# Performance work log

Measured on AMD Instinct MI355X. Metric: run time of the kernel, lower is better.

The kernel has to match this reference:

```python
import jax, jax.numpy as jnp
import numpy as np

EMBED_DIM = 1024
NUM_HEADS = 16
HEAD_DIM = EMBED_DIM // NUM_HEADS
BSZ = 8
SEQ = 1024


def setup_inputs() -> dict:
    key = jax.random.key(0)
    ks = jax.random.split(key, 8)
    s = 1.0 / np.sqrt(EMBED_DIM)
    return {
        "query": jax.random.normal(ks[0], (BSZ, SEQ, EMBED_DIM), jnp.float32),
        "key": jax.random.normal(ks[1], (BSZ, SEQ, EMBED_DIM), jnp.float32),
        "value": jax.random.normal(ks[2], (BSZ, SEQ, EMBED_DIM), jnp.float32),
        "Wq": jax.random.normal(ks[3], (EMBED_DIM, EMBED_DIM), jnp.float32) * s,
        "bq": jnp.zeros((EMBED_DIM,), jnp.float32),
        "Wk": jax.random.normal(ks[4], (EMBED_DIM, EMBED_DIM), jnp.float32) * s,
        "bk": jnp.zeros((EMBED_DIM,), jnp.float32),
        "Wv": jax.random.normal(ks[5], (EMBED_DIM, EMBED_DIM), jnp.float32) * s,
        "bv": jnp.zeros((EMBED_DIM,), jnp.float32),
        "Wo": jax.random.normal(ks[6], (EMBED_DIM, EMBED_DIM), jnp.float32) * s,
        "bo": jnp.zeros((EMBED_DIM,), jnp.float32),
    }


def reference(query, key, value, Wq, bq, Wk, bk, Wv, bv, Wo, bo):
    # B=0 path of hfta MultiheadAttention, dropout=0 (eval), no masks.
    bsz, tgt_len, embed_dim = query.shape
    src_len = key.shape[1]
    scaling = HEAD_DIM ** -0.5

    # torch Linear: y = x @ W.T + b
    q = (jnp.einsum('bte,fe->btf', query, Wq) + bq) * scaling
    k = jnp.einsum('bse,fe->bsf', key, Wk) + bk
    v = jnp.einsum('bse,fe->bsf', value, Wv) + bv

    # split heads: [b, h, t, d]
    q = q.reshape(bsz, tgt_len, NUM_HEADS, HEAD_DIM).transpose(0, 2, 1, 3)
    k = k.reshape(bsz, src_len, NUM_HEADS, HEAD_DIM).transpose(0, 2, 1, 3)
    v = v.reshape(bsz, src_len, NUM_HEADS, HEAD_DIM).transpose(0, 2, 1, 3)

    scores = jnp.einsum('bhtd,bhsd->bhts', q, k)          # [b,h,t,s]
    attn = jax.nn.softmax(scores, axis=-1)
    o = jnp.einsum('bhts,bhsd->bhtd', attn, v)            # [b,h,t,d]
    o = o.transpose(0, 2, 1, 3).reshape(bsz, tgt_len, embed_dim)
    o = jnp.einsum('bte,fe->btf', o, Wo) + bo
    return o
```

## Files before the change

kernel.cpp:

```cpp
#include <hip/hip_runtime.h>
#include <hip/hip_bf16.h>

#define BSZ   8
#define SEQ   1024
#define EMB   1024
#define NH    16
#define HD    64
#define MROWS (BSZ*SEQ)
#define LOG2E 1.44269504088896f

typedef short  short8  __attribute__((ext_vector_type(8)));
typedef short  short4v __attribute__((ext_vector_type(4)));
typedef float  floatx4 __attribute__((ext_vector_type(4)));
typedef unsigned int uint2v __attribute__((ext_vector_type(2)));
typedef unsigned int uint4v __attribute__((ext_vector_type(4)));

__device__ __forceinline__ unsigned short f2bf(float f) {
  union { float f; unsigned u; } v; v.f = f;
  unsigned r = v.u + 0x7FFFu + ((v.u >> 16) & 1u);
  return (unsigned short)(r >> 16);
}
__device__ __forceinline__ unsigned pk2bf(float a, float b) {
  __hip_bfloat162 t = __float22bfloat162_rn(make_float2(a, b));
  union { __hip_bfloat162 h; unsigned u; } c; c.h = t; return c.u;
}

__device__ __forceinline__ void g2lds16(const unsigned short* g, unsigned short* l) {
  __builtin_amdgcn_global_load_lds(
      (const __attribute__((address_space(1))) unsigned int*)g,
      (__attribute__((address_space(3))) unsigned int*)l, 16, 0, 0);
}

__global__ __launch_bounds__(256) void convert_w4(
    const float* __restrict__ w0, const float* __restrict__ w1,
    const float* __restrict__ w2, const float* __restrict__ w3,
    unsigned short* __restrict__ out, float qs)
{
  const int z = blockIdx.y;
  const float* w = (z == 0) ? w0 : (z == 1) ? w1 : (z == 2) ? w2 : w3;
  const float s = (z == 0) ? qs : 1.0f;
  int i = blockIdx.x * 256 + threadIdx.x;
  float4 f = ((const float4*)w)[i];
  short4v p;
  p.x = (short)f2bf(f.x * s); p.y = (short)f2bf(f.y * s);
  p.z = (short)f2bf(f.z * s); p.w = (short)f2bf(f.w * s);
  ((short4v*)(out + (size_t)z * EMB * EMB))[i] = p;
}

template<int QKV>
__global__ __launch_bounds__(256, 2) void gemm_k(
    const float* __restrict__ A0, const float* __restrict__ A1,
    const float* __restrict__ A2,
    const unsigned short* __restrict__ Abf,
    const unsigned short* __restrict__ Wbase,
    const float* __restrict__ b0, const float* __restrict__ b1,
    const float* __restrict__ b2, float qs,
    unsigned short* __restrict__ obf, float* __restrict__ of32)
{
  __shared__ __align__(16) unsigned short As[2][128 * 64];
  __shared__ __align__(16) unsigned short Ws[2][128 * 64];
  const int tid  = threadIdx.x;
  const int lane = tid & 63, wid = tid >> 6;
  const int z    = QKV ? blockIdx.z : 0;
  const int n0   = blockIdx.x * 128;
  const int m0   = blockIdx.y * 128;
  const int wm = (wid & 1) * 64, wn = (wid >> 1) * 64;
  const int quad = lane >> 4, ln = lane & 15, e3 = ln & 7;
  const int lrow = lane >> 3;
  const int lcol8 = ((lane & 7) ^ lrow) * 8;

  const unsigned short* W = Wbase + (size_t)z * EMB * EMB;
  const float* Af = QKV ? ((z == 0) ? A0 : (z == 1) ? A1 : A2) : (const float*)0;
  const int ar = tid >> 1;
  const int ac = (tid & 1) * 32;

  floatx4 acc[4][4] = {};
  float4 ax[8];

  if (QKV) {
    const float* src = Af + (size_t)(m0 + ar) * EMB + ac;
#pragma unroll
    for (int i = 0; i < 8; i++) ax[i] = *(const float4*)(src + i * 4);
  }
#pragma unroll
  for (int c = 0; c < 4; c++) {
    int r = wid * 32 + c * 8;
    g2lds16(W + (size_t)(n0 + r + lrow) * EMB + lcol8, &Ws[0][r * 64]);
    if (!QKV) g2lds16(Abf + (size_t)(m0 + r + lrow) * EMB + lcol8, &As[0][r * 64]);
  }
  if (QKV) {
#pragma unroll
    for (int i = 0; i < 4; i++) {
      uint4v u;
      u.x = pk2bf(ax[2*i].x, ax[2*i].y);     u.y = pk2bf(ax[2*i].z, ax[2*i].w);
      u.z = pk2bf(ax[2*i+1].x, ax[2*i+1].y); u.w = pk2bf(ax[2*i+1].z, ax[2*i+1].w);
      int ch = (4 * (tid & 1) + i) ^ (ar & 7);
      *(uint4v*)&As[0][ar * 64 + ch * 8] = u;
    }
  }

  const int NK = EMB / 64;
  for (int it = 0; it < NK; ++it) {
    __syncthreads();
    const int cb = it & 1, nb = (it + 1) & 1;
    if (it < NK - 1) {
      const int k1 = (it + 1) * 64;
      if (QKV) {
        const float* src = Af + (size_t)(m0 + ar) * EMB + k1 + ac;
#pragma unroll
        for (int i = 0; i < 8; i++) ax[i] = *(const float4*)(src + i * 4);
      }
#pragma unroll
      for (int c = 0; c < 4; c++) {
        int r = wid * 32 + c * 8;
        g2lds16(W + (size_t)(n0 + r + lrow) * EMB + k1 + lcol8, &Ws[nb][r * 64]);
        if (!QKV) g2lds16(Abf + (size_t)(m0 + r + lrow) * EMB + k1 + lcol8, &As[nb][r * 64]);
      }
    }
#pragma unroll
    for (int ks = 0; ks < 2; ks++) {
      short8 af[4], wf[4];
#pragma unroll
      for (int t = 0; t < 4; t++) {
        int pc = ((4 * ks + quad) ^ e3) * 8;
        af[t] = *(const short8*)&As[cb][(wm + t * 16 + ln) * 64 + pc];
        wf[t] = *(const short8*)&Ws[cb][(wn + t * 16 + ln) * 64 + pc];
      }
#pragma unroll
      for (int mi = 0; mi < 4; mi++)
#pragma unroll
        for (int ni = 0; ni < 4; ni++)
          acc[mi][ni] = __builtin_amdgcn_mfma_f32_16x16x32_bf16(
              af[mi], wf[ni], acc[mi][ni], 0, 0, 0);
    }
    if (QKV && it < NK - 1) {
#pragma unroll
      for (int i = 0; i < 4; i++) {
        uint4v u;
        u.x = pk2bf(ax[2*i].x, ax[2*i].y);     u.y = pk2bf(ax[2*i].z, ax[2*i].w);
        u.z = pk2bf(ax[2*i+1].x, ax[2*i+1].y); u.w = pk2bf(ax[2*i+1].z, ax[2*i+1].w);
        int ch = (4 * (tid & 1) + i) ^ (ar & 7);
        *(uint4v*)&As[nb][ar * 64 + ch * 8] = u;
      }
    }
  }

  const float* bias = QKV ? ((z == 0) ? b0 : (z == 1) ? b1 : b2) : b0;
  const float bsc = (QKV && z == 0) ? qs : 1.0f;
  unsigned short* outz = obf + (size_t)z * MROWS * EMB;

#pragma unroll
  for (int mi = 0; mi < 4; mi++) {
#pragma unroll
    for (int ni = 0; ni < 4; ni++) {
      int gn = n0 + wn + ni * 16 + ln;
      float bv = bsc * bias[gn];
      int gmb = m0 + wm + mi * 16 + quad * 4;
      if (!QKV) {
#pragma unroll
        for (int r = 0; r < 4; r++)
          of32[(size_t)(gmb + r) * EMB + gn] = acc[mi][ni][r] + bv;
      } else if (z < 2) {
        int h = gn >> 6, d = gn & 63;
#pragma unroll
        for (int r = 0; r < 4; r++) {
          int gm = gmb + r;
          int b = gm >> 10, s = gm & 1023;
          outz[((size_t)(b * NH + h) * SEQ + s) * HD + d] = f2bf(acc[mi][ni][r] + bv);
        }
      } else {
        int h = gn >> 6, d = gn & 63;
        int b = gmb >> 10, s = gmb & 1023;
        short4v pkt;
        pkt.x = (short)f2bf(acc[mi][ni][0] + bv);
        pkt.y = (short)f2bf(acc[mi][ni][1] + bv);
        pkt.z = (short)f2bf(acc[mi][ni][2] + bv);
        pkt.w = (short)f2bf(acc[mi][ni][3] + bv);
        *(short4v*)&outz[((size_t)(b * NH + h) * HD + d) * SEQ + s] = pkt;
      }
    }
  }
}

__global__ __launch_bounds__(256, 2) void attn_k(
    const unsigned short* __restrict__ q,
    const unsigned short* __restrict__ k,
    const unsigned short* __restrict__ vt,
    unsigned short* __restrict__ o)
{
  __shared__ __align__(16) unsigned short Ks[2][64 * 64];
  __shared__ __align__(16) unsigned short Vs[2][64 * 64];
  __shared__ __align__(16) unsigned short Pb[4][16][72];
  const int tid  = threadIdx.x;
  const int lane = tid & 63, wv = tid >> 6;
  const int quad = lane >> 4, ln = lane & 15, e3 = ln & 7;
  const int bh = blockIdx.x >> 2;
  const int tb = (blockIdx.x & 3) * 256;
  const int b = bh >> 4, h = bh & 15;
  const int lrow = lane >> 3;
  const int lcol8 = ((lane & 7) ^ lrow) * 8;

  const unsigned short* qh = q  + (size_t)bh * SEQ * HD;
  const unsigned short* kh = k  + (size_t)bh * SEQ * HD;
  const unsigned short* vh = vt + (size_t)bh * HD * SEQ;

  short8 qf[4][2];
#pragma unroll
  for (int tt = 0; tt < 4; tt++)
#pragma unroll
    for (int kc = 0; kc < 2; kc++)
      qf[tt][kc] = *(const short8*)(qh +
          (size_t)(tb + tt * 64 + wv * 16 + ln) * HD + kc * 32 + quad * 8);

  const short ONE = (short)0x3F80;
  const short8 onesf = {ONE, ONE, ONE, ONE, ONE, ONE, ONE, ONE};

  floatx4 Oa[4][4] = {};
  floatx4 Ol[4]    = {};

#pragma unroll
  for (int c = 0; c < 2; c++) {
    int ch = wv * 2 + c;
    g2lds16(kh + (size_t)(ch * 8 + lrow) * HD + lcol8,  &Ks[0][ch * 8 * 64]);
    g2lds16(vh + (size_t)(ch * 8 + lrow) * SEQ + lcol8, &Vs[0][ch * 8 * 64]);
  }

  for (int it = 0; it < SEQ / 64; ++it) {
    __syncthreads();
    const int cb = it & 1, nb = (it + 1) & 1;
    if (it < SEQ / 64 - 1) {
      const int s1 = (it + 1) * 64;
#pragma unroll
      for (int c = 0; c < 2; c++) {
        int ch = wv * 2 + c;
        g2lds16(kh + (size_t)(s1 + ch * 8 + lrow) * HD + lcol8,  &Ks[nb][ch * 8 * 64]);
        g2lds16(vh + (size_t)(ch * 8 + lrow) * SEQ + s1 + lcol8, &Vs[nb][ch * 8 * 64]);
      }
    }

    short8 kf[4][2], vf[4][2];
#pragma unroll
    for (int st = 0; st < 4; st++) {
      kf[st][0] = *(const short8*)&Ks[cb][(st * 16 + ln) * 64 + ((0 + quad) ^ e3) * 8];
      kf[st][1] = *(const short8*)&Ks[cb][(st * 16 + ln) * 64 + ((4 + quad) ^ e3) * 8];
      vf[st][0] = *(const short8*)&Vs[cb][(st * 16 + ln) * 64 + ((0 + quad) ^ e3) * 8];
      vf[st][1] = *(const short8*)&Vs[cb][(st * 16 + ln) * 64 + ((4 + quad) ^ e3) * 8];
    }

#pragma unroll
    for (int tt = 0; tt < 4; tt++) {
      floatx4 sc[4];
#pragma unroll
      for (int st = 0; st < 4; st++) {
        floatx4 a = {};
        a = __builtin_amdgcn_mfma_f32_16x16x32_bf16(kf[st][0], qf[tt][0], a, 0, 0, 0);
        a = __builtin_amdgcn_mfma_f32_16x16x32_bf16(kf[st][1], qf[tt][1], a, 0, 0, 0);
        sc[st] = a;
      }
#pragma unroll
      for (int st = 0; st < 4; st++) {
        uint2v u;
        u.x = pk2bf(exp2f(sc[st][0]), exp2f(sc[st][1]));
        u.y = pk2bf(exp2f(sc[st][2]), exp2f(sc[st][3]));
        *(uint2v*)&Pb[wv][ln][st * 16 + quad * 4] = u;
      }
#pragma unroll
      for (int kc = 0; kc < 2; kc++) {
        short8 pf = *(const short8*)&Pb[wv][ln][kc * 32 + quad * 8];
#pragma unroll
        for (int di = 0; di < 4; di++)
          Oa[tt][di] = __builtin_amdgcn_mfma_f32_16x16x32_bf16(vf[di][kc], pf, Oa[tt][di], 0, 0, 0);
        Ol[tt] = __builtin_amdgcn_mfma_f32_16x16x32_bf16(onesf, pf, Ol[tt], 0, 0, 0);
      }
    }
  }

#pragma unroll
  for (int tt = 0; tt < 4; tt++) {
    float linv = 1.0f / Ol[tt][0];
    size_t rowbase = (size_t)(b * SEQ + tb + tt * 64 + wv * 16 + ln) * EMB + h * HD;
#pragma unroll
    for (int di = 0; di < 4; di++) {
      uint2v pkt;
      pkt.x = pk2bf(Oa[tt][di][0] * linv, Oa[tt][di][1] * linv);
      pkt.y = pk2bf(Oa[tt][di][2] * linv, Oa[tt][di][3] * linv);
      *(uint2v*)&o[rowbase + di * 16 + quad * 4] = pkt;
    }
  }
}

extern "C" void kernel_launch(void* const* d_in, const int* in_sizes, int n_in,
                              void* d_out, int out_size, void* d_ws, size_t ws_size,
                              hipStream_t stream) {
  const float* query = (const float*)d_in[0];
  const float* key   = (const float*)d_in[1];
  const float* value = (const float*)d_in[2];
  const float* Wq = (const float*)d_in[3];
  const float* bq = (const float*)d_in[4];
  const float* Wk = (const float*)d_in[5];
  const float* bk = (const float*)d_in[6];
  const float* Wv = (const float*)d_in[7];
  const float* bv = (const float*)d_in[8];
  const float* Wo = (const float*)d_in[9];
  const float* bo = (const float*)d_in[10];
  float* out = (float*)d_out;

  unsigned short* ws = (unsigned short*)d_ws;
  const size_t WSZ = (size_t)EMB * EMB;
  const size_t TSZ = (size_t)MROWS * EMB;
  unsigned short* Wb   = ws;
  unsigned short* q_b  = Wb + 4 * WSZ;
  unsigned short* k_b  = q_b + TSZ;
  unsigned short* vt_b = k_b + TSZ;
  unsigned short* o_b  = vt_b + TSZ;

  const float qscale = 0.125f * LOG2E;

  convert_w4<<<dim3((int)(WSZ / 4 / 256), 4), 256, 0, stream>>>(Wq, Wk, Wv, Wo, Wb, qscale);

  gemm_k<1><<<dim3(EMB / 128, MROWS / 128, 3), 256, 0, stream>>>(
      query, key, value, (const unsigned short*)0, Wb,
      bq, bk, bv, qscale, q_b, (float*)0);

  attn_k<<<dim3(BSZ * NH * (SEQ / 256)), 256, 0, stream>>>(q_b, k_b, vt_b, o_b);

  gemm_k<0><<<dim3(EMB / 128, MROWS / 128, 1), 256, 0, stream>>>(
      (const float*)0, (const float*)0, (const float*)0, o_b, Wb + 3 * WSZ,
      bo, (const float*)0, (const float*)0, 1.0f, (unsigned short*)0, out);
}
```

Before: 388.8 us.

## Remap GEMM and attention blocks for XCD locality, single-buffer GEMM LDS

Flattens the GEMM and attention grids to 1D and remaps block indices so that blocks sharing the same A rows (or the same batch-head) land on the same XCD, which is meant to improve L2 reuse on the multi-die GPU. It also drops the GEMM's double-buffered LDS and register-prefetch pipeline in favour of a simple load-sync-compute-sync loop. This halves GEMM shared memory, which may raise occupancy, but global-load latency is no longer overlapped with the MFMA work.

```diff
diff --git a/kernel.cpp b/kernel.cpp
--- a/kernel.cpp
+++ b/kernel.cpp
@@ -57,13 +57,21 @@
     const float* __restrict__ b2, float qs,
     unsigned short* __restrict__ obf, float* __restrict__ of32)
 {
-  __shared__ __align__(16) unsigned short As[2][128 * 64];
-  __shared__ __align__(16) unsigned short Ws[2][128 * 64];
+  __shared__ __align__(16) unsigned short As[128 * 64];
+  __shared__ __align__(16) unsigned short Ws[128 * 64];
   const int tid  = threadIdx.x;
   const int lane = tid & 63, wid = tid >> 6;
-  const int z    = QKV ? blockIdx.z : 0;
-  const int n0   = blockIdx.x * 128;
-  const int m0   = blockIdx.y * 128;
+
+  const int j    = blockIdx.x;
+  const int xcd  = j & 7;
+  const int rest = j >> 3;
+  const int nb   = rest & 7;
+  int z, mrow;
+  if (QKV) { int mz = rest >> 3; mrow = xcd + 8 * (mz & 7); z = mz >> 3; }
+  else     { mrow = xcd + 8 * (rest >> 3); z = 0; }
+  const int n0 = nb * 128;
+  const int m0 = mrow * 128;
+
   const int wm = (wid & 1) * 64, wn = (wid >> 1) * 64;
   const int quad = lane >> 4, ln = lane & 15, e3 = ln & 7;
   const int lrow = lane >> 3;
@@ -75,56 +83,42 @@
   const int ac = (tid & 1) * 32;
 
   floatx4 acc[4][4] = {};
-  float4 ax[8];
-
-  if (QKV) {
-    const float* src = Af + (size_t)(m0 + ar) * EMB + ac;
-#pragma unroll
-    for (int i = 0; i < 8; i++) ax[i] = *(const float4*)(src + i * 4);
-  }
-#pragma unroll
-  for (int c = 0; c < 4; c++) {
-    int r = wid * 32 + c * 8;
-    g2lds16(W + (size_t)(n0 + r + lrow) * EMB + lcol8, &Ws[0][r * 64]);
-    if (!QKV) g2lds16(Abf + (size_t)(m0 + r + lrow) * EMB + lcol8, &As[0][r * 64]);
-  }
-  if (QKV) {
-#pragma unroll
-    for (int i = 0; i < 4; i++) {
-      uint4v u;
-      u.x = pk2bf(ax[2*i].x, ax[2*i].y);     u.y = pk2bf(ax[2*i].z, ax[2*i].w);
-      u.z = pk2bf(ax[2*i+1].x, ax[2*i+1].y); u.w = pk2bf(ax[2*i+1].z, ax[2*i+1].w);
-      int ch = (4 * (tid & 1) + i) ^ (ar & 7);
-      *(uint4v*)&As[0][ar * 64 + ch * 8] = u;
-    }
-  }
-
-  const int NK = EMB / 64;
-  for (int it = 0; it < NK; ++it) {
-    __syncthreads();
-    const int cb = it & 1, nb = (it + 1) & 1;
-    if (it < NK - 1) {
-      const int k1 = (it + 1) * 64;
-      if (QKV) {
-        const float* src = Af + (size_t)(m0 + ar) * EMB + k1 + ac;
-#pragma unroll
-        for (int i = 0; i < 8; i++) ax[i] = *(const float4*)(src + i * 4);
+
+  for (int k0 = 0; k0 < EMB; k0 += 64) {
+    if (QKV) {
+      const float* src = Af + (size_t)(m0 + ar) * EMB + k0 + ac;
+#pragma unroll
+      for (int i = 0; i < 4; i++) {
+        float4 x = *(const float4*)(src + i * 8);
+        float4 y = *(const float4*)(src + i * 8 + 4);
+        uint4v u;
+        u.x = pk2bf(x.x, x.y); u.y = pk2bf(x.z, x.w);
+        u.z = pk2bf(y.x, y.y); u.w = pk2bf(y.z, y.w);
+        int ch = (4 * (tid & 1) + i) ^ (ar & 7);
+        *(uint4v*)&As[ar * 64 + ch * 8] = u;
       }
 #pragma unroll
       for (int c = 0; c < 4; c++) {
         int r = wid * 32 + c * 8;
-        g2lds16(W + (size_t)(n0 + r + lrow) * EMB + k1 + lcol8, &Ws[nb][r * 64]);
-        if (!QKV) g2lds16(Abf + (size_t)(m0 + r + lrow) * EMB + k1 + lcol8, &As[nb][r * 64]);
-      }
-    }
+        g2lds16(W + (size_t)(n0 + r + lrow) * EMB + k0 + lcol8, &Ws[r * 64]);
+      }
+    } else {
+#pragma unroll
+      for (int c = 0; c < 4; c++) {
+        int r = wid * 32 + c * 8;
+        g2lds16(Abf + (size_t)(m0 + r + lrow) * EMB + k0 + lcol8, &As[r * 64]);
+        g2lds16(W   + (size_t)(n0 + r + lrow) * EMB + k0 + lcol8, &Ws[r * 64]);
+      }
+    }
+    __syncthreads();
 #pragma unroll
     for (int ks = 0; ks < 2; ks++) {
       short8 af[4], wf[4];
 #pragma unroll
       for (int t = 0; t < 4; t++) {
         int pc = ((4 * ks + quad) ^ e3) * 8;
-        af[t] = *(const short8*)&As[cb][(wm + t * 16 + ln) * 64 + pc];
-        wf[t] = *(const short8*)&Ws[cb][(wn + t * 16 + ln) * 64 + pc];
+        af[t] = *(const short8*)&As[(wm + t * 16 + ln) * 64 + pc];
+        wf[t] = *(const short8*)&Ws[(wn + t * 16 + ln) * 64 + pc];
       }
 #pragma unroll
       for (int mi = 0; mi < 4; mi++)
@@ -133,16 +127,7 @@
           acc[mi][ni] = __builtin_amdgcn_mfma_f32_16x16x32_bf16(
               af[mi], wf[ni], acc[mi][ni], 0, 0, 0);
     }
-    if (QKV && it < NK - 1) {
-#pragma unroll
-      for (int i = 0; i < 4; i++) {
-        uint4v u;
-        u.x = pk2bf(ax[2*i].x, ax[2*i].y);     u.y = pk2bf(ax[2*i].z, ax[2*i].w);
-        u.z = pk2bf(ax[2*i+1].x, ax[2*i+1].y); u.w = pk2bf(ax[2*i+1].z, ax[2*i+1].w);
-        int ch = (4 * (tid & 1) + i) ^ (ar & 7);
-        *(uint4v*)&As[nb][ar * 64 + ch * 8] = u;
-      }
-    }
+    __syncthreads();
   }
 
   const float* bias = QKV ? ((z == 0) ? b0 : (z == 1) ? b1 : b2) : b0;
@@ -194,8 +179,12 @@
   const int tid  = threadIdx.x;
   const int lane = tid & 63, wv = tid >> 6;
   const int quad = lane >> 4, ln = lane & 15, e3 = ln & 7;
-  const int bh = blockIdx.x >> 2;
-  const int tb = (blockIdx.x & 3) * 256;
+
+  const int j    = blockIdx.x;
+  const int rest = j >> 3;
+  const int bh   = (j & 7) + 8 * (rest >> 2);
+  const int tb   = (rest & 3) * 256;
+
   const int b = bh >> 4, h = bh & 15;
   const int lrow = lane >> 3;
   const int lcol8 = ((lane & 7) ^ lrow) * 8;
@@ -227,14 +216,14 @@
 
   for (int it = 0; it < SEQ / 64; ++it) {
     __syncthreads();
-    const int cb = it & 1, nb = (it + 1) & 1;
+    const int cb = it & 1, nbuf = (it + 1) & 1;
     if (it < SEQ / 64 - 1) {
       const int s1 = (it + 1) * 64;
 #pragma unroll
       for (int c = 0; c < 2; c++) {
         int ch = wv * 2 + c;
-        g2lds16(kh + (size_t)(s1 + ch * 8 + lrow) * HD + lcol8,  &Ks[nb][ch * 8 * 64]);
-        g2lds16(vh + (size_t)(ch * 8 + lrow) * SEQ + s1 + lcol8, &Vs[nb][ch * 8 * 64]);
+        g2lds16(kh + (size_t)(s1 + ch * 8 + lrow) * HD + lcol8,  &Ks[nbuf][ch * 8 * 64]);
+        g2lds16(vh + (size_t)(ch * 8 + lrow) * SEQ + s1 + lcol8, &Vs[nbuf][ch * 8 * 64]);
       }
     }
 
@@ -318,13 +307,13 @@
 
   convert_w4<<<dim3((int)(WSZ / 4 / 256), 4), 256, 0, stream>>>(Wq, Wk, Wv, Wo, Wb, qscale);
 
-  gemm_k<1><<<dim3(EMB / 128, MROWS / 128, 3), 256, 0, stream>>>(
+  gemm_k<1><<<dim3(8 * 64 * 3), 256, 0, stream>>>(
       query, key, value, (const unsigned short*)0, Wb,
       bq, bk, bv, qscale, q_b, (float*)0);
 
   attn_k<<<dim3(BSZ * NH * (SEQ / 256)), 256, 0, stream>>>(q_b, k_b, vt_b, o_b);
 
-  gemm_k<0><<<dim3(EMB / 128, MROWS / 128, 1), 256, 0, stream>>>(
+  gemm_k<0><<<dim3(8 * 64), 256, 0, stream>>>(
       (const float*)0, (const float*)0, (const float*)0, o_b, Wb + 3 * WSZ,
       bo, (const float*)0, (const float*)0, 1.0f, (unsigned short*)0, out);
 }
```

Measured after the change: 348.5 us. 1.12x faster.
